# Kernel optimization log

Measured on AMD Instinct MI355X. Metric: run time of the kernel, lower is better.

Reference implementation:

```python
import jax, jax.numpy as jnp
import numpy as np

N, E, G = 50000, 400000, 64
IN_C, HID, OUT_C, HEADS = 256, 128, 256, 4
LRELU_SLOPE = 0.2
LN_EPS = 1e-5


def setup_inputs() -> dict:
    key = jax.random.key(0)
    ks = jax.random.split(key, 16)
    d = {}
    d["x"] = jax.random.normal(ks[0], (N, IN_C), dtype=jnp.float32)
    d["edge_index"] = jax.random.randint(ks[1], (2, E), 0, N, dtype=jnp.int32)
    d["batch"] = jnp.sort(jax.random.randint(ks[2], (N,), 0, G, dtype=jnp.int32))
    s1 = 1.0 / np.sqrt(IN_C)
    d["W1"] = jax.random.uniform(ks[3], (IN_C, HEADS * HID), jnp.float32, -s1, s1)
    d["att_src1"] = jax.random.normal(ks[4], (HEADS, HID), jnp.float32) * 0.1
    d["att_dst1"] = jax.random.normal(ks[5], (HEADS, HID), jnp.float32) * 0.1
    d["b1"] = jnp.zeros((HEADS * HID,), jnp.float32)
    d["ln1_g"] = jnp.ones((HEADS * HID,), jnp.float32)
    d["ln1_b"] = jnp.zeros((HEADS * HID,), jnp.float32)
    s2 = 1.0 / np.sqrt(HEADS * HID)
    d["W2"] = jax.random.uniform(ks[6], (HEADS * HID, OUT_C), jnp.float32, -s2, s2)
    d["att_src2"] = jax.random.normal(ks[7], (1, OUT_C), jnp.float32) * 0.1
    d["att_dst2"] = jax.random.normal(ks[8], (1, OUT_C), jnp.float32) * 0.1
    d["b2"] = jnp.zeros((OUT_C,), jnp.float32)
    d["ln2_g"] = jnp.ones((OUT_C,), jnp.float32)
    d["ln2_b"] = jnp.zeros((OUT_C,), jnp.float32)
    return d


def _layernorm(x, g, b):
    mu = jnp.mean(x, axis=-1, keepdims=True)
    var = jnp.mean(jnp.square(x - mu), axis=-1, keepdims=True)
    return (x - mu) * jax.lax.rsqrt(var + LN_EPS) * g + b


def _gat_conv(x, src, dst, W, a_src, a_dst, bias):
    # PyG GATConv (eval mode, dropout inactive), self-loops already in src/dst.
    H, C = a_src.shape
    h = (x @ W).reshape(N, H, C)                       # [N,H,C]
    e_src = jnp.einsum('nhc,hc->nh', h, a_src)          # [N,H]
    e_dst = jnp.einsum('nhc,hc->nh', h, a_dst)
    e = jax.nn.leaky_relu(e_src[src] + e_dst[dst], LRELU_SLOPE)  # [Etot,H]
    m = jax.ops.segment_max(e, dst, num_segments=N)     # segment softmax over incoming edges
    ex = jnp.exp(e - m[dst])
    s = jax.ops.segment_sum(ex, dst, num_segments=N)
    alpha = ex / (s[dst] + 1e-16)                       # [Etot,H]
    msg = h[src] * alpha[:, :, None]                    # [Etot,H,C]
    out = jax.ops.segment_sum(msg, dst, num_segments=N) # [N,H,C]
    return out.reshape(N, H * C) + bias


def reference(x, edge_index, batch, W1, att_src1, att_dst1, b1, ln1_g, ln1_b,
              W2, att_src2, att_dst2, b2, ln2_g, ln2_b):
    loops = jnp.arange(N, dtype=edge_index.dtype)
    src = jnp.concatenate([edge_index[0], loops])
    dst = jnp.concatenate([edge_index[1], loops])
    h = _gat_conv(x, src, dst, W1, att_src1, att_dst1, b1)
    h = _layernorm(h, ln1_g, ln1_b)
    h = jax.nn.relu(h)                                  # dropout is identity in eval
    h = _gat_conv(h, src, dst, W2, att_src2, att_dst2, b2)
    h = _layernorm(h, ln2_g, ln2_b)
    # global_mean_pool over graphs
    sums = jax.ops.segment_sum(h, batch, num_segments=G)
    cnts = jax.ops.segment_sum(jnp.ones((N,), h.dtype), batch, num_segments=G)
    return sums / jnp.maximum(cnts, 1.0)[:, None]
```

## Files before the change

### kernel.cpp

```cpp
#include <hip/hip_runtime.h>
#include <hip/hip_bf16.h>
#include <cstdint>

#define LRELU_SLOPE 0.2f

typedef short bf16x8 __attribute__((ext_vector_type(8)));
typedef float f32x4  __attribute__((ext_vector_type(4)));

__device__ __forceinline__ float b2f(unsigned short u) {
  return __uint_as_float(((unsigned int)u) << 16);
}
__device__ __forceinline__ unsigned short f2b(float f) {
  unsigned int u = __float_as_uint(f);
  return (unsigned short)((u + 0x7fff + ((u >> 16) & 1)) >> 16);
}

__device__ __forceinline__ void gload16(const void* g, void* l) {
  __builtin_amdgcn_global_load_lds(
      (const __attribute__((address_space(1))) unsigned int*)g,
      (__attribute__((address_space(3))) unsigned int*)l, 16, 0, 0);
}

__global__ __launch_bounds__(256)
void prep_x_count(const float* __restrict__ x, unsigned short* __restrict__ o,
                  int M, int Mpad, const int* __restrict__ ei, int E, int Etot,
                  int* __restrict__ count) {
  const int i = blockIdx.x * 256 + threadIdx.x;
  if (i < Mpad * 64) {
    const int row = i >> 6;
    const int c4  = (i & 63) * 4;
    ushort4 v = make_ushort4(0, 0, 0, 0);
    if (row < M) {
      const float4 f = *(const float4*)&x[(size_t)row * 256 + c4];
      v = make_ushort4(f2b(f.x), f2b(f.y), f2b(f.z), f2b(f.w));
    }
    *(ushort4*)&o[(size_t)row * 256 + c4] = v;
  }
  if (i < Etot) {
    const int d = (i < E) ? ei[E + i] : (i - E);
    atomicAdd(&count[d], 1);
  }
}

__global__ __launch_bounds__(256)
void cvt_wts(const float* __restrict__ W1, const float* __restrict__ W2,
             unsigned short* __restrict__ W1T, unsigned short* __restrict__ W2T) {
  int j = blockIdx.x * 256 + threadIdx.x;
  if (j < 512 * 256) {
    const int n = j >> 8, k = j & 255;
    W1T[j] = f2b(W1[(size_t)k * 512 + n]);
  } else {
    j -= 512 * 256;
    const int n = j >> 9, k = j & 511;
    W2T[j] = f2b(W2[(size_t)k * 256 + n]);
  }
}

__global__ __launch_bounds__(256)
void scan_blocksum(const int* __restrict__ count, int* __restrict__ bsum, int Nn) {
  const int i0 = blockIdx.x * 1024 + threadIdx.x * 4;
  int s = 0;
#pragma unroll
  for (int k = 0; k < 4; ++k) { const int i = i0 + k; if (i < Nn) s += count[i]; }
#pragma unroll
  for (int off = 1; off < 64; off <<= 1) s += __shfl_xor(s, off);
  __shared__ int ws[4];
  if ((threadIdx.x & 63) == 0) ws[threadIdx.x >> 6] = s;
  __syncthreads();
  if (threadIdx.x == 0) bsum[blockIdx.x] = ws[0] + ws[1] + ws[2] + ws[3];
}

__global__ __launch_bounds__(64)
void scan_top(const int* __restrict__ bsum, int* __restrict__ boff,
              int* __restrict__ rowptrN, int nb) {
  const int t = threadIdx.x;
  const int v = (t < nb) ? bsum[t] : 0;
  int incl = v;
#pragma unroll
  for (int off = 1; off < 64; off <<= 1) {
    const int u = __shfl_up(incl, off);
    if (t >= off) incl += u;
  }
  if (t < nb) boff[t] = incl - v;
  if (t == 63) *rowptrN = incl;
}

__global__ __launch_bounds__(256)
void scan_apply(const int* __restrict__ count, const int* __restrict__ boff,
                int* __restrict__ rowptr, int* __restrict__ cursor, int Nn) {
  const int t = threadIdx.x;
  const int lane = t & 63;
  const int w = t >> 6;
  const int i0 = blockIdx.x * 1024 + t * 4;
  int c[4]; int s = 0;
#pragma unroll
  for (int k = 0; k < 4; ++k) { const int i = i0 + k; c[k] = (i < Nn) ? count[i] : 0; s += c[k]; }
  int incl = s;
#pragma unroll
  for (int off = 1; off < 64; off <<= 1) {
    const int u = __shfl_up(incl, off);
    if (lane >= off) incl += u;
  }
  __shared__ int ws[4];
  if (lane == 63) ws[w] = incl;
  __syncthreads();
  int woff = 0;
  for (int k = 0; k < w; ++k) woff += ws[k];
  int base = boff[blockIdx.x] + woff + incl - s;
#pragma unroll
  for (int k = 0; k < 4; ++k) {
    const int i = i0 + k;
    if (i < Nn) { rowptr[i] = base; cursor[i] = base; base += c[k]; }
  }
}

__global__ __launch_bounds__(256)
void csr_scatter(const int* __restrict__ ei, int E, int Etot,
                 int* __restrict__ cursor, int* __restrict__ srcs,
                 int* __restrict__ dsts) {
  const int i = blockIdx.x * 256 + threadIdx.x;
  if (i >= Etot) return;
  const int s = (i < E) ? ei[i]     : (i - E);
  const int d = (i < E) ? ei[E + i] : (i - E);
  const int pos = atomicAdd(&cursor[d], 1);
  srcs[pos] = s;
  dsts[pos] = d;
}

template<int KSTEPS>
__global__ __launch_bounds__(256)
void gemm_bf16(const unsigned short* __restrict__ A,
               const unsigned short* __restrict__ BT,
               unsigned short* __restrict__ C, int M, int Nn, int K,
               const float* __restrict__ asrc, const float* __restrict__ adst,
               float* __restrict__ es, float* __restrict__ ed,
               int H, int lgC, int esPart) {
  __shared__ unsigned short As[3][128 * 32];
  __shared__ unsigned short Bs[3][128 * 32];
  const int tid  = threadIdx.x;
  const int lane = tid & 63;
  const int wave = tid >> 6;
  const int wm = wave >> 1, wn = wave & 1;
  const int brow = blockIdx.y * 128;
  const int bcol = blockIdx.x * 128;
  const int srow  = tid >> 2;
  const int sslot = tid & 3;
  const int sswz  = sslot ^ (srow & 3);
  const size_t aBase0 = (size_t)(brow + srow) * K + sswz * 8;
  const size_t aBase1 = (size_t)(brow + 64 + srow) * K + sswz * 8;
  const size_t bBase0 = (size_t)(bcol + srow) * K + sswz * 8;
  const size_t bBase1 = (size_t)(bcol + 64 + srow) * K + sswz * 8;
  const int ldsOff0 = srow * 32 + sslot * 8;
  const int ldsOff1 = (64 + srow) * 32 + sslot * 8;
  es += (size_t)blockIdx.x * esPart;
  ed += (size_t)blockIdx.x * esPart;

  f32x4 acc[4][4] = {};
  const int u   = lane >> 4;
  const int r15 = lane & 15;
  const int sw  = u ^ (r15 & 3);

  auto stage = [&](int buf, int ks) {
    const int k0 = ks * 32;
    gload16(A + aBase0 + k0, &As[buf][ldsOff0]);
    gload16(A + aBase1 + k0, &As[buf][ldsOff1]);
    gload16(BT + bBase0 + k0, &Bs[buf][ldsOff0]);
    gload16(BT + bBase1 + k0, &Bs[buf][ldsOff1]);
  };

  stage(0, 0);
  stage(1, 1);
#pragma unroll
  for (int ks = 0; ks < KSTEPS; ++ks) {
    if (ks + 1 < KSTEPS)
      asm volatile("s_waitcnt vmcnt(4)" ::: "memory");
    else
      asm volatile("s_waitcnt vmcnt(0)" ::: "memory");
    __builtin_amdgcn_s_barrier();
    if (ks + 2 < KSTEPS) stage((ks + 2) % 3, ks + 2);
    const int cur = ks % 3;
    bf16x8 af[4], bfv[4];
#pragma unroll
    for (int m = 0; m < 4; ++m) {
      const int row = wm * 64 + m * 16 + r15;
      af[m]  = *(const bf16x8*)&As[cur][row * 32 + sw * 8];
      const int col = wn * 64 + m * 16 + r15;
      bfv[m] = *(const bf16x8*)&Bs[cur][col * 32 + sw * 8];
    }
#pragma unroll
    for (int m = 0; m < 4; ++m)
#pragma unroll
      for (int n = 0; n < 4; ++n)
        acc[m][n] = __builtin_amdgcn_mfma_f32_16x16x32_bf16(
            af[m], bfv[n], acc[m][n], 0, 0, 0);
  }
#pragma unroll
  for (int m = 0; m < 4; ++m) {
    const int r0 = brow + wm * 64 + m * 16 + u * 4;
#pragma unroll
    for (int n = 0; n < 4; ++n) {
      const int cc = bcol + wn * 64 + n * 16 + r15;
#pragma unroll
      for (int r = 0; r < 4; ++r)
        if (r0 + r < M) C[(size_t)(r0 + r) * Nn + cc] = f2b(acc[m][n][r]);
    }
  }
  const int head = bcol >> lgC;
  float asv[4], adv[4];
#pragma unroll
  for (int n = 0; n < 4; ++n) {
    const int cc = bcol + wn * 64 + n * 16 + r15;
    asv[n] = asrc[cc];
    adv[n] = adst[cc];
  }
#pragma unroll
  for (int m = 0; m < 4; ++m) {
#pragma unroll
    for (int r = 0; r < 4; ++r) {
      float pes = 0.f, ped = 0.f;
#pragma unroll
      for (int n = 0; n < 4; ++n) {
        pes = fmaf(acc[m][n][r], asv[n], pes);
        ped = fmaf(acc[m][n][r], adv[n], ped);
      }
#pragma unroll
      for (int off = 1; off < 16; off <<= 1) {
        pes += __shfl_xor(pes, off);
        ped += __shfl_xor(ped, off);
      }
      if (r15 == 0) {
        const int row = brow + wm * 64 + m * 16 + u * 4 + r;
        if (row < M) {
          unsafeAtomicAdd(&es[row * H + head], pes);
          unsafeAtomicAdd(&ed[row * H + head], ped);
        }
      }
    }
  }
}

template<int H>
__global__ __launch_bounds__(256)
void ex_compute(const int* __restrict__ srcs, const int* __restrict__ dsts,
                const float* __restrict__ es, const float* __restrict__ ed,
                float* __restrict__ exCSR, int Etot, int pN) {
  const int p = blockIdx.x * 256 + threadIdx.x;
  if (p >= Etot) return;
  const int sN = srcs[p], dN = dsts[p];
  if constexpr (H == 4) {
    const float4 a = *(const float4*)&es[sN * 4];
    const float4 b = *(const float4*)&ed[dN * 4];
    float e0 = a.x + b.x, e1 = a.y + b.y, e2 = a.z + b.z, e3 = a.w + b.w;
    e0 = (e0 > 0.f) ? e0 : LRELU_SLOPE * e0;
    e1 = (e1 > 0.f) ? e1 : LRELU_SLOPE * e1;
    e2 = (e2 > 0.f) ? e2 : LRELU_SLOPE * e2;
    e3 = (e3 > 0.f) ? e3 : LRELU_SLOPE * e3;
    *(float4*)&exCSR[p * 4] =
        make_float4(__expf(e0), __expf(e1), __expf(e2), __expf(e3));
  } else {
    float e = (es[sN] + es[pN + sN]) + (ed[dN] + ed[pN + dN]);
    e = (e > 0.f) ? e : LRELU_SLOPE * e;
    exCSR[p] = __expf(e);
  }
}

template<int H, int C, bool RELU, bool BFOUT>
__global__ __launch_bounds__(256)
void gat_agg_ln(const int* __restrict__ rowptr, const int* __restrict__ srcs,
                const float* __restrict__ exCSR,
                const unsigned short* __restrict__ h,
                const float* __restrict__ bias, const float* __restrict__ lng,
                const float* __restrict__ lnb, unsigned short* __restrict__ obf,
                float* __restrict__ of32, int Nn) {
  constexpr int HC = H * C;
  constexpr int F  = HC / 64;
  const int wave = threadIdx.x >> 6;
  const int lane = threadIdx.x & 63;
  const int n = blockIdx.x * 4 + wave;
  if (n >= Nn) return;
  const int beg = rowptr[n];
  const int deg = rowptr[n + 1] - beg;
  const int hl = (lane * F) / C;

  float dsum = 0.f;
  if constexpr (H == 4) {
    for (int it = lane; it < deg * 4; it += 64) dsum += exCSR[beg * 4 + it];
#pragma unroll
    for (int off = 4; off < 64; off <<= 1) dsum += __shfl_xor(dsum, off);
    dsum = __shfl(dsum, hl);
  } else {
    for (int it = lane; it < deg; it += 64) dsum += exCSR[beg + it];
#pragma unroll
    for (int off = 1; off < 64; off <<= 1) dsum += __shfl_xor(dsum, off);
  }
  const float inv_s = 1.0f / (dsum + 1e-16f);

  float acc[F];
#pragma unroll
  for (int i = 0; i < F; ++i) acc[i] = 0.f;

  auto fma_rows = [&](const ushort4* v0, const ushort4* v1, const float* a, int cnt) {
    for (int q = 0; q < cnt; ++q) {
      acc[0] = fmaf(b2f(v0[q].x), a[q], acc[0]);
      acc[1] = fmaf(b2f(v0[q].y), a[q], acc[1]);
      acc[2] = fmaf(b2f(v0[q].z), a[q], acc[2]);
      acc[3] = fmaf(b2f(v0[q].w), a[q], acc[3]);
      if constexpr (F == 8) {
        acc[4] = fmaf(b2f(v1[q].x), a[q], acc[4]);
        acc[5] = fmaf(b2f(v1[q].y), a[q], acc[5]);
        acc[6] = fmaf(b2f(v1[q].z), a[q], acc[6]);
        acc[7] = fmaf(b2f(v1[q].w), a[q], acc[7]);
      }
    }
  };

  int j = 0;
  for (; j + 4 <= deg; j += 4) {
    int s4[4];
    float a4[4];
#pragma unroll
    for (int q = 0; q < 4; ++q) s4[q] = srcs[beg + j + q];
#pragma unroll
    for (int q = 0; q < 4; ++q) a4[q] = exCSR[(beg + j + q) * H + hl] * inv_s;
    ushort4 v0[4], v1[4];
#pragma unroll
    for (int q = 0; q < 4; ++q) {
      const unsigned short* hp = &h[(size_t)s4[q] * HC + lane * F];
      v0[q] = *(const ushort4*)hp;
      if constexpr (F == 8) v1[q] = *(const ushort4*)(hp + 4);
    }
    fma_rows(v0, v1, a4, 4);
  }
  for (; j < deg; ++j) {
    const int src = srcs[beg + j];
    const float a = exCSR[(beg + j) * H + hl] * inv_s;
    const unsigned short* hp = &h[(size_t)src * HC + lane * F];
    ushort4 v0 = *(const ushort4*)hp, v1;
    if constexpr (F == 8) v1 = *(const ushort4*)(hp + 4);
    fma_rows(&v0, &v1, &a, 1);
  }

#pragma unroll
  for (int i = 0; i < F; i += 4) {
    const float4 bb = *(const float4*)&bias[lane * F + i];
    acc[i + 0] += bb.x; acc[i + 1] += bb.y;
    acc[i + 2] += bb.z; acc[i + 3] += bb.w;
  }
  float sum = 0.f, sq = 0.f;
#pragma unroll
  for (int i = 0; i < F; ++i) { sum += acc[i]; sq += acc[i] * acc[i]; }
#pragma unroll
  for (int off = 1; off < 64; off <<= 1) {
    sum += __shfl_xor(sum, off);
    sq  += __shfl_xor(sq, off);
  }
  const float mu  = sum / HC;
  const float var = sq / HC - mu * mu;
  const float r   = rsqrtf(var + 1e-5f);
  float y[F];
#pragma unroll
  for (int i = 0; i < F; i += 4) {
    const float4 gg = *(const float4*)&lng[lane * F + i];
    const float4 bl = *(const float4*)&lnb[lane * F + i];
    y[i + 0] = (acc[i + 0] - mu) * r * gg.x + bl.x;
    y[i + 1] = (acc[i + 1] - mu) * r * gg.y + bl.y;
    y[i + 2] = (acc[i + 2] - mu) * r * gg.z + bl.z;
    y[i + 3] = (acc[i + 3] - mu) * r * gg.w + bl.w;
  }
  if constexpr (RELU) {
#pragma unroll
    for (int i = 0; i < F; ++i) y[i] = fmaxf(y[i], 0.f);
  }
  if constexpr (BFOUT) {
    unsigned short* op = &obf[(size_t)n * HC + lane * F];
    *(ushort4*)op = make_ushort4(f2b(y[0]), f2b(y[1]), f2b(y[2]), f2b(y[3]));
    if constexpr (F == 8)
      *(ushort4*)(op + 4) = make_ushort4(f2b(y[4]), f2b(y[5]), f2b(y[6]), f2b(y[7]));
  } else {
    float* op = &of32[(size_t)n * HC + lane * F];
    *(float4*)op = make_float4(y[0], y[1], y[2], y[3]);
    if constexpr (F == 8)
      *(float4*)(op + 4) = make_float4(y[4], y[5], y[6], y[7]);
  }
}

__global__ __launch_bounds__(256)
void pool_partial(const unsigned short* __restrict__ x, const int* __restrict__ batch,
                  float* __restrict__ tmp, int* __restrict__ cnt, int Nn) {
  const int r0 = blockIdx.x * 64;
  const int rend = min(r0 + 64, Nn);
  const int t = threadIdx.x;
  float acc = 0.f;
  int cur = batch[r0];
  int seglen = 0;
  for (int r = r0; r < rend; ++r) {
    const int g = batch[r];
    if (g != cur) {
      unsafeAtomicAdd(&tmp[cur * 256 + t], acc);
      if (t == 0) atomicAdd(&cnt[cur], seglen);
      acc = 0.f; seglen = 0; cur = g;
    }
    acc += b2f(x[(size_t)r * 256 + t]);
    ++seglen;
  }
  unsafeAtomicAdd(&tmp[cur * 256 + t], acc);
  if (t == 0) atomicAdd(&cnt[cur], seglen);
}

__global__ __launch_bounds__(256)
void pool_final(const float* __restrict__ tmp, const int* __restrict__ cnt,
                float* __restrict__ out) {
  const int g = blockIdx.x;
  const int t = threadIdx.x;
  out[g * 256 + t] = tmp[g * 256 + t] / fmaxf((float)cnt[g], 1.f);
}

extern "C" void kernel_launch(void* const* d_in, const int* in_sizes, int n_in,
                              void* d_out, int out_size, void* d_ws, size_t ws_size,
                              hipStream_t stream) {
  const float* x    = (const float*)d_in[0];
  const int*   ei   = (const int*)d_in[1];
  const int*   batch= (const int*)d_in[2];
  const float* W1   = (const float*)d_in[3];
  const float* as1  = (const float*)d_in[4];
  const float* ad1  = (const float*)d_in[5];
  const float* b1   = (const float*)d_in[6];
  const float* g1   = (const float*)d_in[7];
  const float* be1  = (const float*)d_in[8];
  const float* W2   = (const float*)d_in[9];
  const float* as2  = (const float*)d_in[10];
  const float* ad2  = (const float*)d_in[11];
  const float* b2   = (const float*)d_in[12];
  const float* g2   = (const float*)d_in[13];
  const float* be2  = (const float*)d_in[14];

  const int N    = in_sizes[0] / 256;
  const int E    = in_sizes[1] / 2;
  const int Etot = E + N;
  const int Mpad = ((N + 127) / 128) * 128;
  const int NB   = (N + 1023) / 1024;

  float* ws = (float*)d_ws;
  unsigned short* out2 = (unsigned short*)ws;
  unsigned short* A2bf = out2 + (size_t)N * 256;
  unsigned short* A1bf = A2bf;
  unsigned short* h1bf = A2bf + (size_t)Mpad * 512;
  unsigned short* W1T  = h1bf + (size_t)N * 512;
  unsigned short* W2T  = W1T + 512 * 256;
  float* es1 = (float*)(W2T + 512 * 256);
  float* ed1 = es1 + (size_t)N * 4;
  float* es2 = ed1 + (size_t)N * 4;
  float* ed2 = es2 + (size_t)N * 2;
  int* count  = (int*)(ed2 + (size_t)N * 2);
  int* rowptr = count + N;
  int* cursor = rowptr + N + 4;
  int* srcs   = cursor + N;
  int* dsts   = srcs + Etot;
  float* exCSR = (float*)(dsts + Etot);
  float* ptmp = exCSR + (size_t)Etot * 4;
  int*   pcnt = (int*)(ptmp + 64 * 256);
  int*   bsum = pcnt + 64;
  int*   boff = bsum + 64;
  unsigned short* h2bf = h1bf;

  const int eb = (Etot + 255) / 256;

  hipMemsetAsync(es1, 0, (size_t)N * 13 * 4, stream);
  hipMemsetAsync(ptmp, 0, (size_t)(64 * 256 + 64) * 4, stream);
  hipMemsetAsync(A2bf + (size_t)N * 512, 0, (size_t)(Mpad - N) * 512 * 2, stream);

  prep_x_count<<<(Mpad * 64 + 255) / 256, 256, 0, stream>>>(
      x, A1bf, N, Mpad, ei, E, Etot, count);
  cvt_wts<<<(2 * 512 * 256 + 255) / 256, 256, 0, stream>>>(W1, W2, W1T, W2T);

  scan_blocksum<<<NB, 256, 0, stream>>>(count, bsum, N);
  scan_top<<<1, 64, 0, stream>>>(bsum, boff, &rowptr[N], NB);
  scan_apply<<<NB, 256, 0, stream>>>(count, boff, rowptr, cursor, N);
  csr_scatter<<<eb, 256, 0, stream>>>(ei, E, Etot, cursor, srcs, dsts);

  gemm_bf16<8><<<dim3(4, Mpad / 128), 256, 0, stream>>>(
      A1bf, W1T, h1bf, N, 512, 256, as1, ad1, es1, ed1, 4, 7, 0);
  ex_compute<4><<<eb, 256, 0, stream>>>(srcs, dsts, es1, ed1, exCSR, Etot, 0);
  gat_agg_ln<4, 128, true, true><<<(N + 3) / 4, 256, 0, stream>>>(
      rowptr, srcs, exCSR, h1bf, b1, g1, be1, A2bf, nullptr, N);

  gemm_bf16<16><<<dim3(2, Mpad / 128), 256, 0, stream>>>(
      A2bf, W2T, h2bf, N, 256, 512, as2, ad2, es2, ed2, 1, 8, N);
  ex_compute<1><<<eb, 256, 0, stream>>>(srcs, dsts, es2, ed2, exCSR, Etot, N);
  gat_agg_ln<1, 256, false, true><<<(N + 3) / 4, 256, 0, stream>>>(
      rowptr, srcs, exCSR, h2bf, b2, g2, be2, out2, nullptr, N);

  pool_partial<<<(N + 63) / 64, 256, 0, stream>>>(out2, batch, ptmp, pcnt, N);
  pool_final<<<64, 256, 0, stream>>>(ptmp, pcnt, (float*)d_out);
}
```

Baseline: 333.9 us.

## Make GEMM persistent with XCD-aware tile grouping and continuous cross-tile pipelining

Replaces the 2D grid of one-tile GEMM blocks with a persistent grid (768 or 512 blocks). Each block loops over a contiguous range of row tiles for a fixed column tile, and the grouping by XCD (bid&7) keeps the shared B columns and A rows in the same L2. The triple-buffered load pipeline now runs across tile boundaries, with the epilogue (bf16 store plus attention-logit atomics) done inline after each tile, and the LDS swizzle is changed. This cuts launch and tail overhead and improves cache locality, but it adds a full vmcnt(0) drain at each tile boundary and makes the epilogue serialize with the next tile's compute.

```diff
diff --git a/kernel.cpp b/kernel.cpp
--- a/kernel.cpp
+++ b/kernel.cpp
@@ -127,58 +127,80 @@
   dsts[pos] = d;
 }
 
-template<int KSTEPS>
+template<int KSTEPS, int NBCOL, int GRPX>
 __global__ __launch_bounds__(256)
 void gemm_bf16(const unsigned short* __restrict__ A,
                const unsigned short* __restrict__ BT,
                unsigned short* __restrict__ C, int M, int Nn, int K,
                const float* __restrict__ asrc, const float* __restrict__ adst,
                float* __restrict__ es, float* __restrict__ ed,
-               int H, int lgC, int esPart) {
+               int H, int lgC, int esPart, int TB) {
   __shared__ unsigned short As[3][128 * 32];
   __shared__ unsigned short Bs[3][128 * 32];
   const int tid  = threadIdx.x;
   const int lane = tid & 63;
   const int wave = tid >> 6;
   const int wm = wave >> 1, wn = wave & 1;
-  const int brow = blockIdx.y * 128;
-  const int bcol = blockIdx.x * 128;
+  const int bid = blockIdx.x;
+  const int xcd = bid & 7;
+  const int w   = bid >> 3;
+  const int bcol_t = w % NBCOL;
+  const int grp = xcd * GRPX + w / NBCOL;
+  constexpr int G = 8 * GRPX * 1;
+  const int q = TB / G, r = TB % G;
+  const int t0 = grp * q + min(grp, r);
+  const int nT = q + (grp < r ? 1 : 0);
+  const int bcol = bcol_t * 128;
   const int srow  = tid >> 2;
   const int sslot = tid & 3;
-  const int sswz  = sslot ^ (srow & 3);
-  const size_t aBase0 = (size_t)(brow + srow) * K + sswz * 8;
-  const size_t aBase1 = (size_t)(brow + 64 + srow) * K + sswz * 8;
-  const size_t bBase0 = (size_t)(bcol + srow) * K + sswz * 8;
-  const size_t bBase1 = (size_t)(bcol + 64 + srow) * K + sswz * 8;
+  const int sswz  = sslot ^ ((srow ^ (srow >> 2)) & 3);
   const int ldsOff0 = srow * 32 + sslot * 8;
   const int ldsOff1 = (64 + srow) * 32 + sslot * 8;
-  es += (size_t)blockIdx.x * esPart;
-  ed += (size_t)blockIdx.x * esPart;
-
-  f32x4 acc[4][4] = {};
+  const size_t bB0 = (size_t)(bcol + srow) * K + sswz * 8;
+  const size_t bB1 = (size_t)(bcol + 64 + srow) * K + sswz * 8;
+  es += (size_t)bcol_t * esPart;
+  ed += (size_t)bcol_t * esPart;
   const int u   = lane >> 4;
   const int r15 = lane & 15;
-  const int sw  = u ^ (r15 & 3);
-
-  auto stage = [&](int buf, int ks) {
-    const int k0 = ks * 32;
-    gload16(A + aBase0 + k0, &As[buf][ldsOff0]);
-    gload16(A + aBase1 + k0, &As[buf][ldsOff1]);
-    gload16(BT + bBase0 + k0, &Bs[buf][ldsOff0]);
-    gload16(BT + bBase1 + k0, &Bs[buf][ldsOff1]);
+  const int sw  = u ^ ((r15 ^ (r15 >> 2)) & 3);
+  const int head = bcol >> lgC;
+  float asv[4], adv[4];
+#pragma unroll
+  for (int n = 0; n < 4; ++n) {
+    const int cc = bcol + wn * 64 + n * 16 + r15;
+    asv[n] = asrc[cc];
+    adv[n] = adst[cc];
+  }
+
+  auto stageA = [&](int buf, int tile, int ks) {
+    const size_t base = (size_t)(tile * 128 + srow) * K + sswz * 8 + ks * 32;
+    gload16(A + base, &As[buf][ldsOff0]);
+    gload16(A + base + (size_t)64 * K, &As[buf][ldsOff1]);
   };
-
-  stage(0, 0);
-  stage(1, 1);
-#pragma unroll
-  for (int ks = 0; ks < KSTEPS; ++ks) {
-    if (ks + 1 < KSTEPS)
+  auto stageB = [&](int buf, int ks) {
+    gload16(BT + bB0 + ks * 32, &Bs[buf][ldsOff0]);
+    gload16(BT + bB1 + ks * 32, &Bs[buf][ldsOff1]);
+  };
+
+  const int tot = nT * KSTEPS;
+  stageA(0, t0, 0); stageB(0, 0);
+  stageA(1, t0, 1); stageB(1, 1);
+
+  f32x4 acc[4][4] = {};
+  int cur = 0;
+  for (int vs = 0; vs < tot; ++vs) {
+    const int ks = vs % KSTEPS;
+    if (vs + 1 == tot || (ks == 0 && vs != 0))
+      asm volatile("s_waitcnt vmcnt(0)" ::: "memory");
+    else
       asm volatile("s_waitcnt vmcnt(4)" ::: "memory");
-    else
-      asm volatile("s_waitcnt vmcnt(0)" ::: "memory");
     __builtin_amdgcn_s_barrier();
-    if (ks + 2 < KSTEPS) stage((ks + 2) % 3, ks + 2);
-    const int cur = ks % 3;
+    const int vs2 = vs + 2;
+    if (vs2 < tot) {
+      const int nb = (cur + 2 >= 3) ? cur - 1 : cur + 2;
+      stageA(nb, t0 + vs2 / KSTEPS, vs2 % KSTEPS);
+      stageB(nb, vs2 % KSTEPS);
+    }
     bf16x8 af[4], bfv[4];
 #pragma unroll
     for (int m = 0; m < 4; ++m) {
@@ -193,49 +215,50 @@
       for (int n = 0; n < 4; ++n)
         acc[m][n] = __builtin_amdgcn_mfma_f32_16x16x32_bf16(
             af[m], bfv[n], acc[m][n], 0, 0, 0);
-  }
-#pragma unroll
-  for (int m = 0; m < 4; ++m) {
-    const int r0 = brow + wm * 64 + m * 16 + u * 4;
-#pragma unroll
-    for (int n = 0; n < 4; ++n) {
-      const int cc = bcol + wn * 64 + n * 16 + r15;
-#pragma unroll
-      for (int r = 0; r < 4; ++r)
-        if (r0 + r < M) C[(size_t)(r0 + r) * Nn + cc] = f2b(acc[m][n][r]);
-    }
-  }
-  const int head = bcol >> lgC;
-  float asv[4], adv[4];
-#pragma unroll
-  for (int n = 0; n < 4; ++n) {
-    const int cc = bcol + wn * 64 + n * 16 + r15;
-    asv[n] = asrc[cc];
-    adv[n] = adst[cc];
-  }
-#pragma unroll
-  for (int m = 0; m < 4; ++m) {
-#pragma unroll
-    for (int r = 0; r < 4; ++r) {
-      float pes = 0.f, ped = 0.f;
-#pragma unroll
-      for (int n = 0; n < 4; ++n) {
-        pes = fmaf(acc[m][n][r], asv[n], pes);
-        ped = fmaf(acc[m][n][r], adv[n], ped);
-      }
-#pragma unroll
-      for (int off = 1; off < 16; off <<= 1) {
-        pes += __shfl_xor(pes, off);
-        ped += __shfl_xor(ped, off);
-      }
-      if (r15 == 0) {
-        const int row = brow + wm * 64 + m * 16 + u * 4 + r;
-        if (row < M) {
-          unsafeAtomicAdd(&es[row * H + head], pes);
-          unsafeAtomicAdd(&ed[row * H + head], ped);
+    if (ks == KSTEPS - 1) {
+      const int brow = (t0 + vs / KSTEPS) * 128;
+#pragma unroll
+      for (int m = 0; m < 4; ++m) {
+        const int r0 = brow + wm * 64 + m * 16 + u * 4;
+#pragma unroll
+        for (int n = 0; n < 4; ++n) {
+          const int cc = bcol + wn * 64 + n * 16 + r15;
+#pragma unroll
+          for (int rr = 0; rr < 4; ++rr)
+            if (r0 + rr < M) C[(size_t)(r0 + rr) * Nn + cc] = f2b(acc[m][n][rr]);
         }
       }
-    }
+#pragma unroll
+      for (int m = 0; m < 4; ++m) {
+#pragma unroll
+        for (int rr = 0; rr < 4; ++rr) {
+          float pes = 0.f, ped = 0.f;
+#pragma unroll
+          for (int n = 0; n < 4; ++n) {
+            pes = fmaf(acc[m][n][rr], asv[n], pes);
+            ped = fmaf(acc[m][n][rr], adv[n], ped);
+          }
+#pragma unroll
+          for (int off = 1; off < 16; off <<= 1) {
+            pes += __shfl_xor(pes, off);
+            ped += __shfl_xor(ped, off);
+          }
+          if (r15 == 0) {
+            const int row = brow + wm * 64 + m * 16 + u * 4 + rr;
+            if (row < M) {
+              unsafeAtomicAdd(&es[row * H + head], pes);
+              unsafeAtomicAdd(&ed[row * H + head], ped);
+            }
+          }
+        }
+      }
+#pragma unroll
+      for (int m = 0; m < 4; ++m)
+#pragma unroll
+        for (int n = 0; n < 4; ++n)
+          acc[m][n] = (f32x4){0.f, 0.f, 0.f, 0.f};
+    }
+    cur = (cur + 1 == 3) ? 0 : cur + 1;
   }
 }
 
@@ -438,6 +461,7 @@
   const int E    = in_sizes[1] / 2;
   const int Etot = E + N;
   const int Mpad = ((N + 127) / 128) * 128;
+  const int TB   = Mpad / 128;
   const int NB   = (N + 1023) / 1024;
 
   float* ws = (float*)d_ws;
@@ -478,14 +502,14 @@
   scan_apply<<<NB, 256, 0, stream>>>(count, boff, rowptr, cursor, N);
   csr_scatter<<<eb, 256, 0, stream>>>(ei, E, Etot, cursor, srcs, dsts);
 
-  gemm_bf16<8><<<dim3(4, Mpad / 128), 256, 0, stream>>>(
-      A1bf, W1T, h1bf, N, 512, 256, as1, ad1, es1, ed1, 4, 7, 0);
+  gemm_bf16<8, 4, 24><<<768, 256, 0, stream>>>(
+      A1bf, W1T, h1bf, N, 512, 256, as1, ad1, es1, ed1, 4, 7, 0, TB);
   ex_compute<4><<<eb, 256, 0, stream>>>(srcs, dsts, es1, ed1, exCSR, Etot, 0);
   gat_agg_ln<4, 128, true, true><<<(N + 3) / 4, 256, 0, stream>>>(
       rowptr, srcs, exCSR, h1bf, b1, g1, be1, A2bf, nullptr, N);
 
-  gemm_bf16<16><<<dim3(2, Mpad / 128), 256, 0, stream>>>(
-      A2bf, W2T, h2bf, N, 256, 512, as2, ad2, es2, ed2, 1, 8, N);
+  gemm_bf16<16, 2, 32><<<512, 256, 0, stream>>>(
+      A2bf, W2T, h2bf, N, 256, 512, as2, ad2, es2, ed2, 1, 8, N, TB);
   ex_compute<1><<<eb, 256, 0, stream>>>(srcs, dsts, es2, ed2, exCSR, Etot, N);
   gat_agg_ln<1, 256, false, true><<<(N + 3) / 4, 256, 0, stream>>>(
       rowptr, srcs, exCSR, h2bf, b2, g2, be2, out2, nullptr, N);
```

Measured after the change: 361.8 us. 1.08x slower.

## Keep B tile resident in LDS, stream A from registers, stage C stores

Applied to the files above, without the earlier changes.

The GEMM is replaced by a B-resident design. The whole B tile for the block's column range is loaded into LDS once, and A fragments are streamed straight from global memory into registers with double buffering. This removes the per-k-step barriers and LDS traffic for A. The output goes through LDS so it can be written with coalesced 16-byte stores, and layer 2 uses 256x64 tiles, which needs 4 partial es/ed slices and a wider memset. A loads now come from global memory without LDS sharing, so latency may be exposed.

```diff
diff --git a/kernel.cpp b/kernel.cpp
--- a/kernel.cpp
+++ b/kernel.cpp
@@ -127,84 +127,97 @@
   dsts[pos] = d;
 }
 
-template<int KSTEPS>
-__global__ __launch_bounds__(256)
-void gemm_bf16(const unsigned short* __restrict__ A,
+template<int BM, int BN, int WN, int K2, int KSTEPS>
+__global__ __launch_bounds__(256)
+void gemm_bres(const unsigned short* __restrict__ A,
                const unsigned short* __restrict__ BT,
-               unsigned short* __restrict__ C, int M, int Nn, int K,
+               unsigned short* __restrict__ C, int M, int Nn,
                const float* __restrict__ asrc, const float* __restrict__ adst,
                float* __restrict__ es, float* __restrict__ ed,
                int H, int lgC, int esPart) {
-  __shared__ unsigned short As[3][128 * 32];
-  __shared__ unsigned short Bs[3][128 * 32];
+  __shared__ __align__(16) unsigned char lds[65536];
   const int tid  = threadIdx.x;
   const int lane = tid & 63;
-  const int wave = tid >> 6;
-  const int wm = wave >> 1, wn = wave & 1;
-  const int brow = blockIdx.y * 128;
-  const int bcol = blockIdx.x * 128;
-  const int srow  = tid >> 2;
-  const int sslot = tid & 3;
-  const int sswz  = sslot ^ (srow & 3);
-  const size_t aBase0 = (size_t)(brow + srow) * K + sswz * 8;
-  const size_t aBase1 = (size_t)(brow + 64 + srow) * K + sswz * 8;
-  const size_t bBase0 = (size_t)(bcol + srow) * K + sswz * 8;
-  const size_t bBase1 = (size_t)(bcol + 64 + srow) * K + sswz * 8;
-  const int ldsOff0 = srow * 32 + sslot * 8;
-  const int ldsOff1 = (64 + srow) * 32 + sslot * 8;
+  const int wid  = tid >> 6;
+  const int wm = (WN == 2) ? (wid >> 1) : wid;
+  const int wn = (WN == 2) ? (wid & 1) : 0;
+  const int brow = blockIdx.y * BM;
+  const int bcol = blockIdx.x * BN;
+  const int u = lane >> 4, r15 = lane & 15;
+
+  const char* Bb = (const char*)BT;
+#pragma unroll
+  for (int i = 0; i < 16; ++i) {
+    const int b = (i * 256 + tid) * 16;
+    const int col = b / K2;
+    const int kb = (b & (K2 - 1)) ^ ((col & 7) << 4);
+    gload16(Bb + (size_t)(bcol + col) * K2 + kb, &lds[b]);
+  }
+  const char* aptr[4];
+#pragma unroll
+  for (int m = 0; m < 4; ++m)
+    aptr[m] = (const char*)A +
+              (size_t)(brow + wm * 64 + m * 16 + r15) * K2 + u * 16;
+  int bbase[4], bsc[4];
+#pragma unroll
+  for (int n = 0; n < 4; ++n) {
+    const int col = wn * 64 + n * 16 + r15;
+    bbase[n] = col * K2;
+    bsc[n]   = (col & 7) << 4;
+  }
+  asm volatile("s_waitcnt vmcnt(0)" ::: "memory");
+  __builtin_amdgcn_s_barrier();
+
+  f32x4 acc[4][4] = {};
+  bf16x8 a0[4], a1[4];
+#pragma unroll
+  for (int m = 0; m < 4; ++m) a0[m] = *(const bf16x8*)(aptr[m]);
+#pragma unroll
+  for (int ks = 0; ks < KSTEPS; ++ks) {
+    if (ks + 1 < KSTEPS) {
+#pragma unroll
+      for (int m = 0; m < 4; ++m)
+        ((ks & 1) ? a0 : a1)[m] = *(const bf16x8*)(aptr[m] + (ks + 1) * 64);
+    }
+    bf16x8 bfv[4];
+#pragma unroll
+    for (int n = 0; n < 4; ++n)
+      bfv[n] = *(const bf16x8*)&lds[bbase[n] + ((ks * 64 + u * 16) ^ bsc[n])];
+#pragma unroll
+    for (int m = 0; m < 4; ++m)
+#pragma unroll
+      for (int n = 0; n < 4; ++n)
+        acc[m][n] = __builtin_amdgcn_mfma_f32_16x16x32_bf16(
+            ((ks & 1) ? a1 : a0)[m], bfv[n], acc[m][n], 0, 0, 0);
+  }
+
+  __builtin_amdgcn_s_barrier();
+  constexpr int CP = BN * 2 + 16;
+#pragma unroll
+  for (int m = 0; m < 4; ++m)
+#pragma unroll
+    for (int n = 0; n < 4; ++n) {
+      const int col = wn * 64 + n * 16 + r15;
+#pragma unroll
+      for (int rr = 0; rr < 4; ++rr) {
+        const int row = wm * 64 + m * 16 + u * 4 + rr;
+        *(unsigned short*)&lds[row * CP + col * 2] = f2b(acc[m][n][rr]);
+      }
+    }
+  __builtin_amdgcn_s_barrier();
+#pragma unroll
+  for (int i = 0; i < BM * BN * 2 / (256 * 16); ++i) {
+    const int idx = (i * 256 + tid) * 16;
+    const int row = idx / (BN * 2);
+    const int cb  = idx % (BN * 2);
+    const int grow = brow + row;
+    if (grow < M)
+      *(float4*)((char*)C + ((size_t)grow * Nn + bcol) * 2 + cb) =
+          *(const float4*)&lds[row * CP + cb];
+  }
+
   es += (size_t)blockIdx.x * esPart;
   ed += (size_t)blockIdx.x * esPart;
-
-  f32x4 acc[4][4] = {};
-  const int u   = lane >> 4;
-  const int r15 = lane & 15;
-  const int sw  = u ^ (r15 & 3);
-
-  auto stage = [&](int buf, int ks) {
-    const int k0 = ks * 32;
-    gload16(A + aBase0 + k0, &As[buf][ldsOff0]);
-    gload16(A + aBase1 + k0, &As[buf][ldsOff1]);
-    gload16(BT + bBase0 + k0, &Bs[buf][ldsOff0]);
-    gload16(BT + bBase1 + k0, &Bs[buf][ldsOff1]);
-  };
-
-  stage(0, 0);
-  stage(1, 1);
-#pragma unroll
-  for (int ks = 0; ks < KSTEPS; ++ks) {
-    if (ks + 1 < KSTEPS)
-      asm volatile("s_waitcnt vmcnt(4)" ::: "memory");
-    else
-      asm volatile("s_waitcnt vmcnt(0)" ::: "memory");
-    __builtin_amdgcn_s_barrier();
-    if (ks + 2 < KSTEPS) stage((ks + 2) % 3, ks + 2);
-    const int cur = ks % 3;
-    bf16x8 af[4], bfv[4];
-#pragma unroll
-    for (int m = 0; m < 4; ++m) {
-      const int row = wm * 64 + m * 16 + r15;
-      af[m]  = *(const bf16x8*)&As[cur][row * 32 + sw * 8];
-      const int col = wn * 64 + m * 16 + r15;
-      bfv[m] = *(const bf16x8*)&Bs[cur][col * 32 + sw * 8];
-    }
-#pragma unroll
-    for (int m = 0; m < 4; ++m)
-#pragma unroll
-      for (int n = 0; n < 4; ++n)
-        acc[m][n] = __builtin_amdgcn_mfma_f32_16x16x32_bf16(
-            af[m], bfv[n], acc[m][n], 0, 0, 0);
-  }
-#pragma unroll
-  for (int m = 0; m < 4; ++m) {
-    const int r0 = brow + wm * 64 + m * 16 + u * 4;
-#pragma unroll
-    for (int n = 0; n < 4; ++n) {
-      const int cc = bcol + wn * 64 + n * 16 + r15;
-#pragma unroll
-      for (int r = 0; r < 4; ++r)
-        if (r0 + r < M) C[(size_t)(r0 + r) * Nn + cc] = f2b(acc[m][n][r]);
-    }
-  }
   const int head = bcol >> lgC;
   float asv[4], adv[4];
 #pragma unroll
@@ -216,12 +229,12 @@
 #pragma unroll
   for (int m = 0; m < 4; ++m) {
 #pragma unroll
-    for (int r = 0; r < 4; ++r) {
+    for (int rr = 0; rr < 4; ++rr) {
       float pes = 0.f, ped = 0.f;
 #pragma unroll
       for (int n = 0; n < 4; ++n) {
-        pes = fmaf(acc[m][n][r], asv[n], pes);
-        ped = fmaf(acc[m][n][r], adv[n], ped);
+        pes = fmaf(acc[m][n][rr], asv[n], pes);
+        ped = fmaf(acc[m][n][rr], adv[n], ped);
       }
 #pragma unroll
       for (int off = 1; off < 16; off <<= 1) {
@@ -229,7 +242,7 @@
         ped += __shfl_xor(ped, off);
       }
       if (r15 == 0) {
-        const int row = brow + wm * 64 + m * 16 + u * 4 + r;
+        const int row = brow + wm * 64 + m * 16 + u * 4 + rr;
         if (row < M) {
           unsafeAtomicAdd(&es[row * H + head], pes);
           unsafeAtomicAdd(&ed[row * H + head], ped);
@@ -258,7 +271,10 @@
     *(float4*)&exCSR[p * 4] =
         make_float4(__expf(e0), __expf(e1), __expf(e2), __expf(e3));
   } else {
-    float e = (es[sN] + es[pN + sN]) + (ed[dN] + ed[pN + dN]);
+    float se = 0.f, de = 0.f;
+#pragma unroll
+    for (int q = 0; q < 4; ++q) { se += es[q * pN + sN]; de += ed[q * pN + dN]; }
+    float e = se + de;
     e = (e > 0.f) ? e : LRELU_SLOPE * e;
     exCSR[p] = __expf(e);
   }
@@ -437,7 +453,7 @@
   const int N    = in_sizes[0] / 256;
   const int E    = in_sizes[1] / 2;
   const int Etot = E + N;
-  const int Mpad = ((N + 127) / 128) * 128;
+  const int Mpad = ((N + 255) / 256) * 256;
   const int NB   = (N + 1023) / 1024;
 
   float* ws = (float*)d_ws;
@@ -450,8 +466,8 @@
   float* es1 = (float*)(W2T + 512 * 256);
   float* ed1 = es1 + (size_t)N * 4;
   float* es2 = ed1 + (size_t)N * 4;
-  float* ed2 = es2 + (size_t)N * 2;
-  int* count  = (int*)(ed2 + (size_t)N * 2);
+  float* ed2 = es2 + (size_t)N * 4;
+  int* count  = (int*)(ed2 + (size_t)N * 4);
   int* rowptr = count + N;
   int* cursor = rowptr + N + 4;
   int* srcs   = cursor + N;
@@ -465,7 +481,7 @@
 
   const int eb = (Etot + 255) / 256;
 
-  hipMemsetAsync(es1, 0, (size_t)N * 13 * 4, stream);
+  hipMemsetAsync(es1, 0, (size_t)N * 17 * 4, stream);
   hipMemsetAsync(ptmp, 0, (size_t)(64 * 256 + 64) * 4, stream);
   hipMemsetAsync(A2bf + (size_t)N * 512, 0, (size_t)(Mpad - N) * 512 * 2, stream);
 
@@ -478,14 +494,14 @@
   scan_apply<<<NB, 256, 0, stream>>>(count, boff, rowptr, cursor, N);
   csr_scatter<<<eb, 256, 0, stream>>>(ei, E, Etot, cursor, srcs, dsts);
 
-  gemm_bf16<8><<<dim3(4, Mpad / 128), 256, 0, stream>>>(
-      A1bf, W1T, h1bf, N, 512, 256, as1, ad1, es1, ed1, 4, 7, 0);
+  gemm_bres<128, 128, 2, 512, 8><<<dim3(4, Mpad / 128), 256, 0, stream>>>(
+      A1bf, W1T, h1bf, N, 512, as1, ad1, es1, ed1, 4, 7, 0);
   ex_compute<4><<<eb, 256, 0, stream>>>(srcs, dsts, es1, ed1, exCSR, Etot, 0);
   gat_agg_ln<4, 128, true, true><<<(N + 3) / 4, 256, 0, stream>>>(
       rowptr, srcs, exCSR, h1bf, b1, g1, be1, A2bf, nullptr, N);
 
-  gemm_bf16<16><<<dim3(2, Mpad / 128), 256, 0, stream>>>(
-      A2bf, W2T, h2bf, N, 256, 512, as2, ad2, es2, ed2, 1, 8, N);
+  gemm_bres<256, 64, 1, 1024, 16><<<dim3(4, Mpad / 256), 256, 0, stream>>>(
+      A2bf, W2T, h2bf, N, 256, as2, ad2, es2, ed2, 1, 8, N);
   ex_compute<1><<<eb, 256, 0, stream>>>(srcs, dsts, es2, ed2, exCSR, Etot, N);
   gat_agg_ln<1, 256, false, true><<<(N + 3) / 4, 256, 0, stream>>>(
       rowptr, srcs, exCSR, h2bf, b2, g2, be2, out2, nullptr, N);
```

Result: slower. 353.1 us (+5.7%).

## Shrink GEMM tile to 64x128, double-buffer, and stage output through LDS

Applied to the files above, without the earlier changes.

The bf16 GEMM now uses a 64-row by 128-column block tile in place of 128x128, doubling the number of blocks on the row axis to improve occupancy and CU coverage for the tall-skinny matrices. The K-loop switches from a triple-buffered pipeline with partial vmcnt waits to a simpler double buffer with a full wait and barrier each step. The epilogue writes the tile to LDS and then issues coalesced 16-byte stores in place of scattered 2-byte stores. In exchange it gets less B-operand reuse per block, weaker load/compute overlap, and more barriers.

```diff
diff --git a/kernel.cpp b/kernel.cpp
--- a/kernel.cpp
+++ b/kernel.cpp
@@ -135,76 +135,92 @@
                const float* __restrict__ asrc, const float* __restrict__ adst,
                float* __restrict__ es, float* __restrict__ ed,
                int H, int lgC, int esPart) {
-  __shared__ unsigned short As[3][128 * 32];
-  __shared__ unsigned short Bs[3][128 * 32];
+  __shared__ __align__(16) unsigned short smA[2][64 * 32];
+  __shared__ __align__(16) unsigned short smB[2][128 * 32];
   const int tid  = threadIdx.x;
   const int lane = tid & 63;
-  const int wave = tid >> 6;
-  const int wm = wave >> 1, wn = wave & 1;
-  const int brow = blockIdx.y * 128;
+  const int wid  = tid >> 6;
+  const int wm = wid >> 1, wn = wid & 1;
+  const int brow = blockIdx.y * 64;
   const int bcol = blockIdx.x * 128;
-  const int srow  = tid >> 2;
-  const int sslot = tid & 3;
-  const int sswz  = sslot ^ (srow & 3);
-  const size_t aBase0 = (size_t)(brow + srow) * K + sswz * 8;
-  const size_t aBase1 = (size_t)(brow + 64 + srow) * K + sswz * 8;
-  const size_t bBase0 = (size_t)(bcol + srow) * K + sswz * 8;
-  const size_t bBase1 = (size_t)(bcol + 64 + srow) * K + sswz * 8;
-  const int ldsOff0 = srow * 32 + sslot * 8;
-  const int ldsOff1 = (64 + srow) * 32 + sslot * 8;
-  es += (size_t)blockIdx.x * esPart;
-  ed += (size_t)blockIdx.x * esPart;
-
-  f32x4 acc[4][4] = {};
-  const int u   = lane >> 4;
-  const int r15 = lane & 15;
-  const int sw  = u ^ (r15 & 3);
+  const int u = lane >> 4, r15 = lane & 15;
+  const int arow = tid >> 2, aslot = tid & 3;
+  const size_t aBase = (size_t)(brow + arow) * K + (aslot ^ (arow & 3)) * 8;
+  const int ldsA = arow * 32 + aslot * 8;
+  const int brow0 = tid >> 2,        bslot0 = tid & 3;
+  const int brow1 = (256 + tid) >> 2, bslot1 = tid & 3;
+  const size_t bBase0 = (size_t)(bcol + brow0) * K + (bslot0 ^ (brow0 & 3)) * 8;
+  const size_t bBase1 = (size_t)(bcol + brow1) * K + (bslot1 ^ (brow1 & 3)) * 8;
+  const int ldsB0 = brow0 * 32 + bslot0 * 8;
+  const int ldsB1 = brow1 * 32 + bslot1 * 8;
 
   auto stage = [&](int buf, int ks) {
     const int k0 = ks * 32;
-    gload16(A + aBase0 + k0, &As[buf][ldsOff0]);
-    gload16(A + aBase1 + k0, &As[buf][ldsOff1]);
-    gload16(BT + bBase0 + k0, &Bs[buf][ldsOff0]);
-    gload16(BT + bBase1 + k0, &Bs[buf][ldsOff1]);
+    gload16(A + aBase + k0, &smA[buf][ldsA]);
+    gload16(BT + bBase0 + k0, &smB[buf][ldsB0]);
+    gload16(BT + bBase1 + k0, &smB[buf][ldsB1]);
   };
 
+  f32x4 acc[2][4] = {};
+  const int sw = u ^ (r15 & 3);
+
   stage(0, 0);
-  stage(1, 1);
+  asm volatile("s_waitcnt vmcnt(0)" ::: "memory");
+  __syncthreads();
+  int cur = 0;
 #pragma unroll
   for (int ks = 0; ks < KSTEPS; ++ks) {
-    if (ks + 1 < KSTEPS)
-      asm volatile("s_waitcnt vmcnt(4)" ::: "memory");
-    else
-      asm volatile("s_waitcnt vmcnt(0)" ::: "memory");
-    __builtin_amdgcn_s_barrier();
-    if (ks + 2 < KSTEPS) stage((ks + 2) % 3, ks + 2);
-    const int cur = ks % 3;
-    bf16x8 af[4], bfv[4];
-#pragma unroll
-    for (int m = 0; m < 4; ++m) {
-      const int row = wm * 64 + m * 16 + r15;
-      af[m]  = *(const bf16x8*)&As[cur][row * 32 + sw * 8];
-      const int col = wn * 64 + m * 16 + r15;
-      bfv[m] = *(const bf16x8*)&Bs[cur][col * 32 + sw * 8];
-    }
-#pragma unroll
-    for (int m = 0; m < 4; ++m)
+    if (ks + 1 < KSTEPS) stage(cur ^ 1, ks + 1);
+    bf16x8 af[2], bfv[4];
+#pragma unroll
+    for (int m = 0; m < 2; ++m) {
+      const int row = wm * 32 + m * 16 + r15;
+      af[m] = *(const bf16x8*)&smA[cur][row * 32 + sw * 8];
+    }
+#pragma unroll
+    for (int n = 0; n < 4; ++n) {
+      const int col = wn * 64 + n * 16 + r15;
+      bfv[n] = *(const bf16x8*)&smB[cur][col * 32 + sw * 8];
+    }
+#pragma unroll
+    for (int m = 0; m < 2; ++m)
 #pragma unroll
       for (int n = 0; n < 4; ++n)
         acc[m][n] = __builtin_amdgcn_mfma_f32_16x16x32_bf16(
             af[m], bfv[n], acc[m][n], 0, 0, 0);
-  }
-#pragma unroll
-  for (int m = 0; m < 4; ++m) {
-    const int r0 = brow + wm * 64 + m * 16 + u * 4;
+    if (ks + 1 < KSTEPS) {
+      asm volatile("s_waitcnt vmcnt(0)" ::: "memory");
+      __syncthreads();
+      cur ^= 1;
+    }
+  }
+
+  __syncthreads();
+  unsigned short* cb = &smB[0][0];
+#pragma unroll
+  for (int m = 0; m < 2; ++m)
 #pragma unroll
     for (int n = 0; n < 4; ++n) {
-      const int cc = bcol + wn * 64 + n * 16 + r15;
-#pragma unroll
-      for (int r = 0; r < 4; ++r)
-        if (r0 + r < M) C[(size_t)(r0 + r) * Nn + cc] = f2b(acc[m][n][r]);
-    }
-  }
+      const int col = wn * 64 + n * 16 + r15;
+#pragma unroll
+      for (int rr = 0; rr < 4; ++rr) {
+        const int row = wm * 32 + m * 16 + u * 4 + rr;
+        cb[row * 128 + col] = f2b(acc[m][n][rr]);
+      }
+    }
+  __syncthreads();
+#pragma unroll
+  for (int i = 0; i < 4; ++i) {
+    const int idx = (i * 256 + tid) * 8;
+    const int row = idx >> 7;
+    const int cc  = idx & 127;
+    const int grow = brow + row;
+    if (grow < M)
+      *(float4*)&C[(size_t)grow * Nn + bcol + cc] = *(const float4*)&cb[idx];
+  }
+
+  es += (size_t)blockIdx.x * esPart;
+  ed += (size_t)blockIdx.x * esPart;
   const int head = bcol >> lgC;
   float asv[4], adv[4];
 #pragma unroll
@@ -214,14 +230,14 @@
     adv[n] = adst[cc];
   }
 #pragma unroll
-  for (int m = 0; m < 4; ++m) {
-#pragma unroll
-    for (int r = 0; r < 4; ++r) {
+  for (int m = 0; m < 2; ++m) {
+#pragma unroll
+    for (int rr = 0; rr < 4; ++rr) {
       float pes = 0.f, ped = 0.f;
 #pragma unroll
       for (int n = 0; n < 4; ++n) {
-        pes = fmaf(acc[m][n][r], asv[n], pes);
-        ped = fmaf(acc[m][n][r], adv[n], ped);
+        pes = fmaf(acc[m][n][rr], asv[n], pes);
+        ped = fmaf(acc[m][n][rr], adv[n], ped);
       }
 #pragma unroll
       for (int off = 1; off < 16; off <<= 1) {
@@ -229,7 +245,7 @@
         ped += __shfl_xor(ped, off);
       }
       if (r15 == 0) {
-        const int row = brow + wm * 64 + m * 16 + u * 4 + r;
+        const int row = brow + wm * 32 + m * 16 + u * 4 + rr;
         if (row < M) {
           unsafeAtomicAdd(&es[row * H + head], pes);
           unsafeAtomicAdd(&ed[row * H + head], ped);
@@ -437,7 +453,7 @@
   const int N    = in_sizes[0] / 256;
   const int E    = in_sizes[1] / 2;
   const int Etot = E + N;
-  const int Mpad = ((N + 127) / 128) * 128;
+  const int Mpad = ((N + 63) / 64) * 64;
   const int NB   = (N + 1023) / 1024;
 
   float* ws = (float*)d_ws;
@@ -478,13 +494,13 @@
   scan_apply<<<NB, 256, 0, stream>>>(count, boff, rowptr, cursor, N);
   csr_scatter<<<eb, 256, 0, stream>>>(ei, E, Etot, cursor, srcs, dsts);
 
-  gemm_bf16<8><<<dim3(4, Mpad / 128), 256, 0, stream>>>(
+  gemm_bf16<8><<<dim3(4, Mpad / 64), 256, 0, stream>>>(
       A1bf, W1T, h1bf, N, 512, 256, as1, ad1, es1, ed1, 4, 7, 0);
   ex_compute<4><<<eb, 256, 0, stream>>>(srcs, dsts, es1, ed1, exCSR, Etot, 0);
   gat_agg_ln<4, 128, true, true><<<(N + 3) / 4, 256, 0, stream>>>(
       rowptr, srcs, exCSR, h1bf, b1, g1, be1, A2bf, nullptr, N);
 
-  gemm_bf16<16><<<dim3(2, Mpad / 128), 256, 0, stream>>>(
+  gemm_bf16<16><<<dim3(2, Mpad / 64), 256, 0, stream>>>(
       A2bf, W2T, h2bf, N, 256, 512, as2, ad2, es2, ed2, 1, 8, N);
   ex_compute<1><<<eb, 256, 0, stream>>>(srcs, dsts, es2, ed2, exCSR, Etot, N);
   gat_agg_ln<1, 256, false, true><<<(N + 3) / 4, 256, 0, stream>>>(
```

After: 319.2 us. 4.4% less time.
